# Kernel optimization log

Hardware: AMD Instinct MI355X
Metric: run time of the kernel (lower is better)

Reference implementation:

```python
import jax, jax.numpy as jnp
import numpy as np

MAT_MODE = ((0, 1), (0, 2), (1, 2))
VEC_MODE = (2, 1, 0)
DENSITY_SHIFT = -10.0
DISTANCE_SCALE = 25.0


def grid_sample_2d(img, coords):
    # img: [C, H, W]; coords: [N, 2] in [-1, 1], (x indexes W, y indexes H);
    # bilinear, align_corners=True (matches F.grid_sample in the source).
    C, H, W = img.shape
    x = (coords[:, 0] + 1.0) * 0.5 * (W - 1)
    y = (coords[:, 1] + 1.0) * 0.5 * (H - 1)
    x0 = jnp.floor(x)
    y0 = jnp.floor(y)
    wx = x - x0
    wy = y - y0
    x0i = jnp.clip(x0.astype(jnp.int32), 0, W - 1)
    x1i = jnp.clip(x0i + 1, 0, W - 1)
    y0i = jnp.clip(y0.astype(jnp.int32), 0, H - 1)
    y1i = jnp.clip(y0i + 1, 0, H - 1)
    v00 = img[:, y0i, x0i]
    v01 = img[:, y0i, x1i]
    v10 = img[:, y1i, x0i]
    v11 = img[:, y1i, x1i]
    return (v00 * (1 - wx) * (1 - wy) + v01 * wx * (1 - wy)
            + v10 * (1 - wx) * wy + v11 * wx * wy)  # [C, N]


def line_sample_1d(line, t):
    # line: [C, L]; t: [N] in [-1, 1]. Equivalent to the source's grid_sample on a
    # [1, C, L, 1] tensor with coords (0, t): the width dim (size 1) collapses.
    C, L = line.shape
    y = (t + 1.0) * 0.5 * (L - 1)
    y0 = jnp.floor(y)
    wy = y - y0
    y0i = jnp.clip(y0.astype(jnp.int32), 0, L - 1)
    y1i = jnp.clip(y0i + 1, 0, L - 1)
    return line[:, y0i] * (1 - wy) + line[:, y1i] * wy  # [C, N]


def tensorf_features(planes, lines, xyz):
    # planes: [3, C, H, W]; lines: [3, C, L]; xyz: [N, 3] normalized coords.
    # fusion_two='concat' then fusion_one='multiply' == per-plane multiply, concat.
    feats = []
    for i in range(3):
        a, b = MAT_MODE[i]
        pc = jnp.stack([xyz[:, a], xyz[:, b]], axis=-1)  # [N, 2]
        pf = grid_sample_2d(planes[i], pc)               # [C, N]
        lf = line_sample_1d(lines[i], xyz[:, VEC_MODE[i]])  # [C, N]
        feats.append(pf * lf)
    return jnp.concatenate(feats, axis=0)  # [3C, N]


def raw2alpha(sigma, dist):
    # sigma, dist: [Nr, Ns]
    alpha = 1.0 - jnp.exp(-sigma * dist)
    T = jnp.cumprod(jnp.concatenate(
        [jnp.ones((alpha.shape[0], 1), alpha.dtype), 1.0 - alpha + 1e-10], axis=-1), axis=-1)
    weights = alpha * T[:, :-1]
    return alpha, weights, T[:, -1:]


def setup_inputs() -> dict:
    key = jax.random.key(0)
    ks = jax.random.split(key, 10)
    Nr, Ns, G = 4096, 256, 300
    aabb = jnp.array([[-1.5, -1.5, -1.5], [1.5, 1.5, 1.5]], jnp.float32)
    xyz_sampled = jax.random.uniform(ks[0], (Nr, Ns, 3), jnp.float32,
                                     minval=-1.5, maxval=1.5)
    vd = jax.random.normal(ks[1], (Nr, 3), jnp.float32)
    viewdirs = vd / jnp.linalg.norm(vd, axis=-1, keepdims=True)
    near, far = 2.0, 6.0
    t = jnp.linspace(0.0, 1.0, Ns, dtype=jnp.float32)
    z_vals = near * (1.0 - t) + far * t
    z_vals = jnp.broadcast_to(z_vals, (Nr, Ns)) + \
        jax.random.uniform(ks[2], (Nr, Ns), jnp.float32) * ((far - near) / Ns)
    z_vals = jnp.sort(z_vals, axis=-1)
    s = 0.1  # init_scale
    return {
        'xyz_sampled': xyz_sampled,
        'viewdirs': viewdirs,
        'z_vals': z_vals,
        'density_planes': s * jax.random.normal(ks[3], (3, 8, G, G), jnp.float32),
        'density_lines': s * jax.random.normal(ks[4], (3, 8, G), jnp.float32),
        'app_planes': s * jax.random.normal(ks[5], (3, 24, G, G), jnp.float32),
        'app_lines': s * jax.random.normal(ks[6], (3, 24, G), jnp.float32),
        'density_basis_w': jnp.ones((1, 24), jnp.float32),  # source inits to 1/density_dim
        'app_basis_w': s * jax.random.normal(ks[7], (3, 72), jnp.float32),
        'aabb': aabb,
    }


def reference(xyz_sampled, viewdirs, z_vals, density_planes, density_lines,
              app_planes, app_lines, density_basis_w, app_basis_w, aabb):
    Nr, Ns, _ = xyz_sampled.shape
    # normalize_coord: map aabb -> [-1, 1]
    inv_size = 2.0 / (aabb[1] - aabb[0])
    xyz = ((xyz_sampled - aabb[0]) * inv_size - 1.0).reshape(-1, 3)  # [N, 3]

    dfeat = tensorf_features(density_planes, density_lines, xyz)      # [24, N]
    sigma_feat = (density_basis_w @ dfeat).reshape(Nr, Ns)            # basis_mat
    sigma = jax.nn.softplus(sigma_feat + DENSITY_SHIFT)               # fea2denseAct

    # ray-marching distances
    dists = z_vals[:, 1:] - z_vals[:, :-1]
    dists = jnp.concatenate([dists, dists[:, -1:]], axis=-1)
    alpha, weights, bg_T = raw2alpha(sigma, dists * DISTANCE_SCALE)

    # appearance branch: RGBRender is identity on the 3-dim basis output
    afeat = tensorf_features(app_planes, app_lines, xyz)              # [72, N]
    rgb = (app_basis_w @ afeat).T.reshape(Nr, Ns, 3)

    rgb_map = jnp.sum(weights[..., None] * rgb, axis=1)               # [Nr, 3]
    return rgb_map
```

## Files before the change

### kernel.cpp

```cpp
#include <hip/hip_runtime.h>
#include <math.h>

#define G  300
#define NS 256
#define NR 4096
#define CT 32

typedef _Float16 half16_t;
typedef _Float16 h8 __attribute__((ext_vector_type(8)));

__global__ __launch_bounds__(256) void prep_planes(
    const float* __restrict__ dp, const float* __restrict__ ap,
    half16_t* __restrict__ out)
{
  int t = blockIdx.x * blockDim.x + threadIdx.x;
  if (t >= 3 * G * G) return;
  int x  = t % G;
  int yi = t / G;
  int y  = yi % G;
  int i  = yi / G;
  const float* dpp = dp + ((size_t)(i * 8) * G + y) * G + x;
  const float* app = ap + ((size_t)(i * 24) * G + y) * G + x;
  h8 v[4];
#pragma unroll
  for (int c = 0; c < 8; ++c) v[c >> 3][c & 7] = (half16_t)dpp[(size_t)c * G * G];
#pragma unroll
  for (int c = 0; c < 24; ++c) {
    int cc = c + 8;
    v[cc >> 3][cc & 7] = (half16_t)app[(size_t)c * G * G];
  }
  h8* o = (h8*)(out + (size_t)t * CT);
#pragma unroll
  for (int m = 0; m < 4; ++m) o[m] = v[m];
}

__global__ __launch_bounds__(256) void prep_lines(
    const float* __restrict__ dl, const float* __restrict__ al,
    half16_t* __restrict__ out)
{
  int t = blockIdx.x * blockDim.x + threadIdx.x;
  if (t >= 3 * G) return;
  int p = t % G;
  int i = t / G;
  h8 v[4];
#pragma unroll
  for (int c = 0; c < 8; ++c) v[c >> 3][c & 7] = (half16_t)dl[(i * 8 + c) * G + p];
#pragma unroll
  for (int c = 0; c < 24; ++c) {
    int cc = c + 8;
    v[cc >> 3][cc & 7] = (half16_t)al[(i * 24 + c) * G + p];
  }
  h8* o = (h8*)(out + (size_t)t * CT);
#pragma unroll
  for (int m = 0; m < 4; ++m) o[m] = v[m];
}

__global__ __launch_bounds__(256) void tensorf_fused(
    const float* __restrict__ xyz, const float* __restrict__ zv,
    const half16_t* __restrict__ planes, const half16_t* __restrict__ lns,
    const float* __restrict__ dbw, const float* __restrict__ abw,
    const float* __restrict__ aabb, float* __restrict__ out)
{
  __shared__ float4 srgb[4][NS];

  const int wv   = threadIdx.x >> 6;
  const int lane = threadIdx.x & 63;
  const int ray  = (blockIdx.x << 2) + wv;
  const int q    = lane >> 2;
  const int r    = lane & 3;

  float W[3][24];
  if (r == 0) {
#pragma unroll
    for (int m = 0; m < 24; ++m) { W[0][m] = dbw[m]; W[1][m] = 0.f; W[2][m] = 0.f; }
  } else {
#pragma unroll
    for (int j = 0; j < 3; ++j)
#pragma unroll
      for (int i = 0; i < 3; ++i)
#pragma unroll
        for (int k = 0; k < 8; ++k)
          W[j][i * 8 + k] = abw[j * 72 + i * 24 + (r - 1) * 8 + k];
  }

  const float a0x = aabb[0], a0y = aabb[1], a0z = aabb[2];
  const float ivx = 2.f / (aabb[3] - aabb[0]);
  const float ivy = 2.f / (aabb[4] - aabb[1]);
  const float ivz = 2.f / (aabb[5] - aabb[2]);

  const int MA[3] = {0, 0, 1};
  const int MB[3] = {1, 2, 2};
  const int MV[3] = {2, 1, 0};

  const int ro = r * 8;

  for (int it = 0; it < NS / 16; ++it) {
    int s = it * 16 + q;
    const float* xp = xyz + ((size_t)ray * NS + s) * 3;
    float g[3];
    g[0] = (xp[0] - a0x) * ivx - 1.f;
    g[1] = (xp[1] - a0y) * ivy - 1.f;
    g[2] = (xp[2] - a0z) * ivz - 1.f;

    float acc0 = 0.f, acc1 = 0.f, acc2 = 0.f;
#pragma unroll
    for (int i = 0; i < 3; ++i) {
      float fx = (g[MA[i]] + 1.f) * (0.5f * (G - 1));
      float fy = (g[MB[i]] + 1.f) * (0.5f * (G - 1));
      float ft = (g[MV[i]] + 1.f) * (0.5f * (G - 1));
      float x0f = floorf(fx), y0f = floorf(fy), t0f = floorf(ft);
      float wx = fx - x0f, wy = fy - y0f, wt = ft - t0f;
      int x0 = min(max((int)x0f, 0), G - 1);
      int y0 = min(max((int)y0f, 0), G - 1);
      int t0 = min(max((int)t0f, 0), G - 1);
      int x1 = min(x0 + 1, G - 1);
      int y1 = min(y0 + 1, G - 1);
      int t1 = min(t0 + 1, G - 1);

      const half16_t* pb = planes + (size_t)i * G * G * CT;
      h8 t00 = *(const h8*)(pb + ((size_t)(y0 * G + x0)) * CT + ro);
      h8 t01 = *(const h8*)(pb + ((size_t)(y0 * G + x1)) * CT + ro);
      h8 t10 = *(const h8*)(pb + ((size_t)(y1 * G + x0)) * CT + ro);
      h8 t11 = *(const h8*)(pb + ((size_t)(y1 * G + x1)) * CT + ro);
      const half16_t* lb = lns + (size_t)i * G * CT + ro;
      h8 l0 = *(const h8*)(lb + (size_t)t0 * CT);
      h8 l1 = *(const h8*)(lb + (size_t)t1 * CT);

      float w00 = (1.f - wx) * (1.f - wy), w01 = wx * (1.f - wy);
      float w10 = (1.f - wx) * wy,         w11 = wx * wy;
      float wl0 = 1.f - wt;
#pragma unroll
      for (int k = 0; k < 8; ++k) {
        float pf = (float)t00[k] * w00 + (float)t01[k] * w01
                 + (float)t10[k] * w10 + (float)t11[k] * w11;
        float lf = (float)l0[k] * wl0 + (float)l1[k] * wt;
        float f  = pf * lf;
        acc0 += W[0][i * 8 + k] * f;
        acc1 += W[1][i * 8 + k] * f;
        acc2 += W[2][i * 8 + k] * f;
      }
    }
    float4 v;
    v.x = (r == 0) ? acc0 : 0.f;
    v.y = (r == 0) ? 0.f : acc0;
    v.z = (r == 0) ? 0.f : acc1;
    v.w = (r == 0) ? 0.f : acc2;
#pragma unroll
    for (int m = 1; m <= 2; m <<= 1) {
      v.x += __shfl_xor(v.x, m);
      v.y += __shfl_xor(v.y, m);
      v.z += __shfl_xor(v.z, m);
      v.w += __shfl_xor(v.w, m);
    }
    if (r == 0) srgb[wv][s] = v;
  }
  __syncthreads();

  const float* zp = zv + (size_t)ray * NS + lane * 4;
  float4 z4 = *(const float4*)zp;
  float znext = __shfl_down(z4.x, 1);
  float d[4];
  d[0] = z4.y - z4.x;
  d[1] = z4.z - z4.y;
  d[2] = z4.w - z4.z;
  d[3] = (lane == 63) ? d[2] : (znext - z4.w);

  float4 c[4];
  float al[4];
  float tl = 1.f;
#pragma unroll
  for (int j = 0; j < 4; ++j) {
    c[j] = srgb[wv][lane * 4 + j];
    float vs = c[j].x - 10.0f;
    float sp = (vs > 0.f) ? (vs + log1pf(expf(-vs))) : log1pf(expf(vs));
    al[j] = 1.f - expf(-sp * (d[j] * 25.0f));
    tl *= (1.f - al[j] + 1e-10f);
  }
  float incl = tl;
#pragma unroll
  for (int off = 1; off < 64; off <<= 1) {
    float p = __shfl_up(incl, off);
    if (lane >= off) incl *= p;
  }
  float T = __shfl_up(incl, 1);
  if (lane == 0) T = 1.f;

  float ar = 0.f, ag = 0.f, ab = 0.f;
#pragma unroll
  for (int j = 0; j < 4; ++j) {
    float w = al[j] * T;
    ar += w * c[j].y;
    ag += w * c[j].z;
    ab += w * c[j].w;
    T *= (1.f - al[j] + 1e-10f);
  }
#pragma unroll
  for (int off = 32; off > 0; off >>= 1) {
    ar += __shfl_down(ar, off);
    ag += __shfl_down(ag, off);
    ab += __shfl_down(ab, off);
  }
  if (lane == 0) {
    out[ray * 3 + 0] = ar;
    out[ray * 3 + 1] = ag;
    out[ray * 3 + 2] = ab;
  }
}

extern "C" void kernel_launch(void* const* d_in, const int* in_sizes, int n_in,
                              void* d_out, int out_size, void* d_ws, size_t ws_size,
                              hipStream_t stream)
{
  const float* xyz  = (const float*)d_in[0];
  const float* zv   = (const float*)d_in[2];
  const float* dp   = (const float*)d_in[3];
  const float* dl   = (const float*)d_in[4];
  const float* ap   = (const float*)d_in[5];
  const float* al   = (const float*)d_in[6];
  const float* dbw  = (const float*)d_in[7];
  const float* abw  = (const float*)d_in[8];
  const float* aabb = (const float*)d_in[9];
  float* out = (float*)d_out;

  half16_t* planes16 = (half16_t*)d_ws;
  half16_t* lines16  = planes16 + (size_t)3 * G * G * CT;

  hipLaunchKernelGGL(prep_planes, dim3((3 * G * G + 255) / 256), dim3(256), 0, stream,
                     dp, ap, planes16);
  hipLaunchKernelGGL(prep_lines, dim3((3 * G + 255) / 256), dim3(256), 0, stream,
                     dl, al, lines16);
  hipLaunchKernelGGL(tensorf_fused, dim3(NR / 4), dim3(256), 0, stream,
                     xyz, zv, planes16, lines16, dbw, abw, aabb, out);
}
```

Baseline: 237.8 us.

## Split rays across two waves, move basis weights to LDS, merge prep kernels

The two prep kernels are merged into one launch. The main kernel now assigns each ray to two wavefronts, each covering half the samples, and doubles the grid. The 72-float per-thread basis weight array moves into shared memory to cut register pressure, with a launch-bounds occupancy hint added. The transmittance scan is stitched across the two halves through shared memory, which costs extra block barriers and LDS traffic.

```diff
diff --git a/kernel.cpp b/kernel.cpp
--- a/kernel.cpp
+++ b/kernel.cpp
@@ -9,79 +9,78 @@
 typedef _Float16 half16_t;
 typedef _Float16 h8 __attribute__((ext_vector_type(8)));
 
-__global__ __launch_bounds__(256) void prep_planes(
+__global__ __launch_bounds__(256) void prep_all(
     const float* __restrict__ dp, const float* __restrict__ ap,
-    half16_t* __restrict__ out)
+    const float* __restrict__ dl, const float* __restrict__ al,
+    half16_t* __restrict__ outp, half16_t* __restrict__ outl)
 {
   int t = blockIdx.x * blockDim.x + threadIdx.x;
-  if (t >= 3 * G * G) return;
-  int x  = t % G;
-  int yi = t / G;
-  int y  = yi % G;
-  int i  = yi / G;
-  const float* dpp = dp + ((size_t)(i * 8) * G + y) * G + x;
-  const float* app = ap + ((size_t)(i * 24) * G + y) * G + x;
-  h8 v[4];
-#pragma unroll
-  for (int c = 0; c < 8; ++c) v[c >> 3][c & 7] = (half16_t)dpp[(size_t)c * G * G];
-#pragma unroll
-  for (int c = 0; c < 24; ++c) {
-    int cc = c + 8;
-    v[cc >> 3][cc & 7] = (half16_t)app[(size_t)c * G * G];
-  }
-  h8* o = (h8*)(out + (size_t)t * CT);
-#pragma unroll
-  for (int m = 0; m < 4; ++m) o[m] = v[m];
+  if (t < 3 * G * G) {
+    int x  = t % G;
+    int yi = t / G;
+    int y  = yi % G;
+    int i  = yi / G;
+    const float* dpp = dp + ((size_t)(i * 8) * G + y) * G + x;
+    const float* app = ap + ((size_t)(i * 24) * G + y) * G + x;
+    h8 v[4];
+#pragma unroll
+    for (int c = 0; c < 8; ++c) v[c >> 3][c & 7] = (half16_t)dpp[(size_t)c * G * G];
+#pragma unroll
+    for (int c = 0; c < 24; ++c) {
+      int cc = c + 8;
+      v[cc >> 3][cc & 7] = (half16_t)app[(size_t)c * G * G];
+    }
+    h8* o = (h8*)(outp + (size_t)t * CT);
+#pragma unroll
+    for (int m = 0; m < 4; ++m) o[m] = v[m];
+  } else {
+    int u = t - 3 * G * G;
+    if (u < 3 * G) {
+      int p = u % G;
+      int i = u / G;
+      h8 v[4];
+#pragma unroll
+      for (int c = 0; c < 8; ++c) v[c >> 3][c & 7] = (half16_t)dl[(i * 8 + c) * G + p];
+#pragma unroll
+      for (int c = 0; c < 24; ++c) {
+        int cc = c + 8;
+        v[cc >> 3][cc & 7] = (half16_t)al[(i * 24 + c) * G + p];
+      }
+      h8* o = (h8*)(outl + (size_t)u * CT);
+#pragma unroll
+      for (int m = 0; m < 4; ++m) o[m] = v[m];
+    }
+  }
 }
 
-__global__ __launch_bounds__(256) void prep_lines(
-    const float* __restrict__ dl, const float* __restrict__ al,
-    half16_t* __restrict__ out)
-{
-  int t = blockIdx.x * blockDim.x + threadIdx.x;
-  if (t >= 3 * G) return;
-  int p = t % G;
-  int i = t / G;
-  h8 v[4];
-#pragma unroll
-  for (int c = 0; c < 8; ++c) v[c >> 3][c & 7] = (half16_t)dl[(i * 8 + c) * G + p];
-#pragma unroll
-  for (int c = 0; c < 24; ++c) {
-    int cc = c + 8;
-    v[cc >> 3][cc & 7] = (half16_t)al[(i * 24 + c) * G + p];
-  }
-  h8* o = (h8*)(out + (size_t)t * CT);
-#pragma unroll
-  for (int m = 0; m < 4; ++m) o[m] = v[m];
-}
-
-__global__ __launch_bounds__(256) void tensorf_fused(
+__global__ __launch_bounds__(256, 7) void tensorf_fused(
     const float* __restrict__ xyz, const float* __restrict__ zv,
     const half16_t* __restrict__ planes, const half16_t* __restrict__ lns,
     const float* __restrict__ dbw, const float* __restrict__ abw,
     const float* __restrict__ aabb, float* __restrict__ out)
 {
-  __shared__ float4 srgb[4][NS];
-
-  const int wv   = threadIdx.x >> 6;
-  const int lane = threadIdx.x & 63;
-  const int ray  = (blockIdx.x << 2) + wv;
+  __shared__ float4 srgb[2][NS];
+  __shared__ float  sW[3][128];
+  __shared__ float  sTot[2];
+  __shared__ float4 sSum[2][2];
+
+  const int tid = threadIdx.x;
+  for (int idx = tid; idx < 3 * 128; idx += 256) {
+    int j = idx >> 7, c = idx & 127;
+    float v = 0.f;
+    if (c < 72) v = abw[j * 72 + c];
+    else if (j == 0 && c < 96) v = dbw[c - 72];
+    sW[j][c] = v;
+  }
+  __syncthreads();
+
+  const int wv   = tid >> 6;
+  const int lane = tid & 63;
+  const int rl   = wv >> 1;
+  const int hf   = wv & 1;
+  const int ray  = (blockIdx.x << 1) + rl;
   const int q    = lane >> 2;
   const int r    = lane & 3;
-
-  float W[3][24];
-  if (r == 0) {
-#pragma unroll
-    for (int m = 0; m < 24; ++m) { W[0][m] = dbw[m]; W[1][m] = 0.f; W[2][m] = 0.f; }
-  } else {
-#pragma unroll
-    for (int j = 0; j < 3; ++j)
-#pragma unroll
-      for (int i = 0; i < 3; ++i)
-#pragma unroll
-        for (int k = 0; k < 8; ++k)
-          W[j][i * 8 + k] = abw[j * 72 + i * 24 + (r - 1) * 8 + k];
-  }
 
   const float a0x = aabb[0], a0y = aabb[1], a0z = aabb[2];
   const float ivx = 2.f / (aabb[3] - aabb[0]);
@@ -94,8 +93,8 @@
 
   const int ro = r * 8;
 
-  for (int it = 0; it < NS / 16; ++it) {
-    int s = it * 16 + q;
+  for (int it = 0; it < 8; ++it) {
+    int s = (hf << 7) + (it << 4) + q;
     const float* xp = xyz + ((size_t)ray * NS + s) * 3;
     float g[3];
     g[0] = (xp[0] - a0x) * ivx - 1.f;
@@ -129,16 +128,30 @@
       float w00 = (1.f - wx) * (1.f - wy), w01 = wx * (1.f - wy);
       float w10 = (1.f - wx) * wy,         w11 = wx * wy;
       float wl0 = 1.f - wt;
+
+      float f[8];
 #pragma unroll
       for (int k = 0; k < 8; ++k) {
         float pf = (float)t00[k] * w00 + (float)t01[k] * w01
                  + (float)t10[k] * w10 + (float)t11[k] * w11;
         float lf = (float)l0[k] * wl0 + (float)l1[k] * wt;
-        float f  = pf * lf;
-        acc0 += W[0][i * 8 + k] * f;
-        acc1 += W[1][i * 8 + k] * f;
-        acc2 += W[2][i * 8 + k] * f;
+        f[k] = pf * lf;
       }
+
+      int cb = (r == 0) ? (72 + i * 8) : (i * 24 + (r - 1) * 8);
+      const float4* wp0 = (const float4*)&sW[0][cb];
+      const float4* wp1 = (const float4*)&sW[1][cb];
+      const float4* wp2 = (const float4*)&sW[2][cb];
+      float4 wa, wb;
+      wa = wp0[0]; wb = wp0[1];
+      acc0 += wa.x * f[0] + wa.y * f[1] + wa.z * f[2] + wa.w * f[3]
+            + wb.x * f[4] + wb.y * f[5] + wb.z * f[6] + wb.w * f[7];
+      wa = wp1[0]; wb = wp1[1];
+      acc1 += wa.x * f[0] + wa.y * f[1] + wa.z * f[2] + wa.w * f[3]
+            + wb.x * f[4] + wb.y * f[5] + wb.z * f[6] + wb.w * f[7];
+      wa = wp2[0]; wb = wp2[1];
+      acc2 += wa.x * f[0] + wa.y * f[1] + wa.z * f[2] + wa.w * f[3]
+            + wb.x * f[4] + wb.y * f[5] + wb.z * f[6] + wb.w * f[7];
     }
     float4 v;
     v.x = (r == 0) ? acc0 : 0.f;
@@ -152,58 +165,65 @@
       v.z += __shfl_xor(v.z, m);
       v.w += __shfl_xor(v.w, m);
     }
-    if (r == 0) srgb[wv][s] = v;
-  }
-  __syncthreads();
-
-  const float* zp = zv + (size_t)ray * NS + lane * 4;
-  float4 z4 = *(const float4*)zp;
-  float znext = __shfl_down(z4.x, 1);
-  float d[4];
-  d[0] = z4.y - z4.x;
-  d[1] = z4.z - z4.y;
-  d[2] = z4.w - z4.z;
-  d[3] = (lane == 63) ? d[2] : (znext - z4.w);
-
-  float4 c[4];
-  float al[4];
-  float tl = 1.f;
-#pragma unroll
-  for (int j = 0; j < 4; ++j) {
-    c[j] = srgb[wv][lane * 4 + j];
-    float vs = c[j].x - 10.0f;
-    float sp = (vs > 0.f) ? (vs + log1pf(expf(-vs))) : log1pf(expf(vs));
-    al[j] = 1.f - expf(-sp * (d[j] * 25.0f));
-    tl *= (1.f - al[j] + 1e-10f);
-  }
+    if (r == 0) srgb[rl][s] = v;
+  }
+  __syncthreads();
+
+  const int s0 = (hf << 7) + (lane << 1);
+  const float* zp = zv + (size_t)ray * NS + s0;
+  float2 z2 = *(const float2*)zp;
+  float d0 = z2.y - z2.x;
+  float d1 = (s0 + 2 < NS) ? (zp[2] - z2.y) : d0;
+
+  float4 c0 = srgb[rl][s0];
+  float4 c1 = srgb[rl][s0 + 1];
+
+  float vs0 = c0.x - 10.0f;
+  float sp0 = (vs0 > 0.f) ? (vs0 + log1pf(expf(-vs0))) : log1pf(expf(vs0));
+  float al0 = 1.f - expf(-sp0 * (d0 * 25.0f));
+  float vs1 = c1.x - 10.0f;
+  float sp1 = (vs1 > 0.f) ? (vs1 + log1pf(expf(-vs1))) : log1pf(expf(vs1));
+  float al1 = 1.f - expf(-sp1 * (d1 * 25.0f));
+
+  float tl = (1.f - al0 + 1e-10f) * (1.f - al1 + 1e-10f);
+
   float incl = tl;
 #pragma unroll
   for (int off = 1; off < 64; off <<= 1) {
     float p = __shfl_up(incl, off);
     if (lane >= off) incl *= p;
   }
-  float T = __shfl_up(incl, 1);
-  if (lane == 0) T = 1.f;
-
-  float ar = 0.f, ag = 0.f, ab = 0.f;
-#pragma unroll
-  for (int j = 0; j < 4; ++j) {
-    float w = al[j] * T;
-    ar += w * c[j].y;
-    ag += w * c[j].z;
-    ab += w * c[j].w;
-    T *= (1.f - al[j] + 1e-10f);
-  }
+  float Twave = __shfl_up(incl, 1);
+  if (lane == 0) Twave = 1.f;
+
+  if (hf == 0 && lane == 63) sTot[rl] = incl;
+  __syncthreads();
+
+  float Tstart = hf ? sTot[rl] : 1.f;
+  float T = Tstart * Twave;
+
+  float w0 = al0 * T;
+  T *= (1.f - al0 + 1e-10f);
+  float w1 = al1 * T;
+
+  float ar = w0 * c0.y + w1 * c1.y;
+  float ag = w0 * c0.z + w1 * c1.z;
+  float ab = w0 * c0.w + w1 * c1.w;
 #pragma unroll
   for (int off = 32; off > 0; off >>= 1) {
     ar += __shfl_down(ar, off);
     ag += __shfl_down(ag, off);
     ab += __shfl_down(ab, off);
   }
-  if (lane == 0) {
-    out[ray * 3 + 0] = ar;
-    out[ray * 3 + 1] = ag;
-    out[ray * 3 + 2] = ab;
+  if (lane == 0) sSum[rl][hf] = make_float4(ar, ag, ab, 0.f);
+  __syncthreads();
+
+  if (hf == 0 && lane == 0) {
+    float4 A = sSum[rl][0];
+    float4 B = sSum[rl][1];
+    out[ray * 3 + 0] = A.x + B.x;
+    out[ray * 3 + 1] = A.y + B.y;
+    out[ray * 3 + 2] = A.z + B.z;
   }
 }
 
@@ -225,10 +245,8 @@
   half16_t* planes16 = (half16_t*)d_ws;
   half16_t* lines16  = planes16 + (size_t)3 * G * G * CT;
 
-  hipLaunchKernelGGL(prep_planes, dim3((3 * G * G + 255) / 256), dim3(256), 0, stream,
-                     dp, ap, planes16);
-  hipLaunchKernelGGL(prep_lines, dim3((3 * G + 255) / 256), dim3(256), 0, stream,
-                     dl, al, lines16);
-  hipLaunchKernelGGL(tensorf_fused, dim3(NR / 4), dim3(256), 0, stream,
+  hipLaunchKernelGGL(prep_all, dim3((3 * G * G + 3 * G + 255) / 256), dim3(256), 0, stream,
+                     dp, ap, dl, al, planes16, lines16);
+  hipLaunchKernelGGL(tensorf_fused, dim3(NR / 2), dim3(256), 0, stream,
                      xyz, zv, planes16, lines16, dbw, abw, aabb, out);
 }
```

Result: slower. 795.5 us (+234.5%).

## Bucket samples into plane row slabs per ray to improve gather locality

Applied to the files above, without the earlier changes.

Each wavefront now sorts its ray's samples into row slabs of each plane, using ballot and popcount into shared-memory lists. It then processes the samples plane by plane and slab by slab, accumulating partial features into shared memory. The aim is to make concurrent gathers across waves hit nearby plane rows and improve cache reuse. This costs sorting overhead, extra LDS traffic, read-modify-write accumulation and uneven loop trip counts. The change also merges the two prep kernels into one launch and moves basis weights into shared memory.

```diff
diff --git a/kernel.cpp b/kernel.cpp
--- a/kernel.cpp
+++ b/kernel.cpp
@@ -5,54 +5,53 @@
 #define NS 256
 #define NR 4096
 #define CT 32
+#define SLABS 4
 
 typedef _Float16 half16_t;
 typedef _Float16 h8 __attribute__((ext_vector_type(8)));
 
-__global__ __launch_bounds__(256) void prep_planes(
+__global__ __launch_bounds__(256) void prep_all(
     const float* __restrict__ dp, const float* __restrict__ ap,
-    half16_t* __restrict__ out)
+    const float* __restrict__ dl, const float* __restrict__ al,
+    half16_t* __restrict__ outp, half16_t* __restrict__ outl)
 {
   int t = blockIdx.x * blockDim.x + threadIdx.x;
-  if (t >= 3 * G * G) return;
-  int x  = t % G;
-  int yi = t / G;
-  int y  = yi % G;
-  int i  = yi / G;
-  const float* dpp = dp + ((size_t)(i * 8) * G + y) * G + x;
-  const float* app = ap + ((size_t)(i * 24) * G + y) * G + x;
-  h8 v[4];
-#pragma unroll
-  for (int c = 0; c < 8; ++c) v[c >> 3][c & 7] = (half16_t)dpp[(size_t)c * G * G];
-#pragma unroll
-  for (int c = 0; c < 24; ++c) {
-    int cc = c + 8;
-    v[cc >> 3][cc & 7] = (half16_t)app[(size_t)c * G * G];
-  }
-  h8* o = (h8*)(out + (size_t)t * CT);
-#pragma unroll
-  for (int m = 0; m < 4; ++m) o[m] = v[m];
-}
-
-__global__ __launch_bounds__(256) void prep_lines(
-    const float* __restrict__ dl, const float* __restrict__ al,
-    half16_t* __restrict__ out)
-{
-  int t = blockIdx.x * blockDim.x + threadIdx.x;
-  if (t >= 3 * G) return;
-  int p = t % G;
-  int i = t / G;
-  h8 v[4];
-#pragma unroll
-  for (int c = 0; c < 8; ++c) v[c >> 3][c & 7] = (half16_t)dl[(i * 8 + c) * G + p];
-#pragma unroll
-  for (int c = 0; c < 24; ++c) {
-    int cc = c + 8;
-    v[cc >> 3][cc & 7] = (half16_t)al[(i * 24 + c) * G + p];
-  }
-  h8* o = (h8*)(out + (size_t)t * CT);
-#pragma unroll
-  for (int m = 0; m < 4; ++m) o[m] = v[m];
+  if (t < 3 * G * G) {
+    int x  = t % G;
+    int yi = t / G;
+    int y  = yi % G;
+    int i  = yi / G;
+    const float* dpp = dp + ((size_t)(i * 8) * G + y) * G + x;
+    const float* app = ap + ((size_t)(i * 24) * G + y) * G + x;
+    h8 v[4];
+#pragma unroll
+    for (int c = 0; c < 8; ++c) v[c >> 3][c & 7] = (half16_t)dpp[(size_t)c * G * G];
+#pragma unroll
+    for (int c = 0; c < 24; ++c) {
+      int cc = c + 8;
+      v[cc >> 3][cc & 7] = (half16_t)app[(size_t)c * G * G];
+    }
+    h8* o = (h8*)(outp + (size_t)t * CT);
+#pragma unroll
+    for (int m = 0; m < 4; ++m) o[m] = v[m];
+  } else {
+    int u = t - 3 * G * G;
+    if (u < 3 * G) {
+      int p = u % G;
+      int i = u / G;
+      h8 v[4];
+#pragma unroll
+      for (int c = 0; c < 8; ++c) v[c >> 3][c & 7] = (half16_t)dl[(i * 8 + c) * G + p];
+#pragma unroll
+      for (int c = 0; c < 24; ++c) {
+        int cc = c + 8;
+        v[cc >> 3][cc & 7] = (half16_t)al[(i * 24 + c) * G + p];
+      }
+      h8* o = (h8*)(outl + (size_t)u * CT);
+#pragma unroll
+      for (int m = 0; m < 4; ++m) o[m] = v[m];
+    }
+  }
 }
 
 __global__ __launch_bounds__(256) void tensorf_fused(
@@ -62,101 +61,162 @@
     const float* __restrict__ aabb, float* __restrict__ out)
 {
   __shared__ float4 srgb[4][NS];
-
-  const int wv   = threadIdx.x >> 6;
-  const int lane = threadIdx.x & 63;
+  __shared__ unsigned char lst[4][2][SLABS][NS];
+  __shared__ float sW[3][128];
+
+  const int tid = threadIdx.x;
+  for (int idx = tid; idx < 3 * 128; idx += 256) {
+    int j = idx >> 7, c = idx & 127;
+    float v = 0.f;
+    if (c < 72) v = abw[j * 72 + c];
+    else if (j == 0 && c < 96) v = dbw[c - 72];
+    sW[j][c] = v;
+  }
+
+  const int wv   = tid >> 6;
+  const int lane = tid & 63;
   const int ray  = (blockIdx.x << 2) + wv;
   const int q    = lane >> 2;
   const int r    = lane & 3;
 
-  float W[3][24];
-  if (r == 0) {
-#pragma unroll
-    for (int m = 0; m < 24; ++m) { W[0][m] = dbw[m]; W[1][m] = 0.f; W[2][m] = 0.f; }
-  } else {
-#pragma unroll
-    for (int j = 0; j < 3; ++j)
-#pragma unroll
-      for (int i = 0; i < 3; ++i)
-#pragma unroll
-        for (int k = 0; k < 8; ++k)
-          W[j][i * 8 + k] = abw[j * 72 + i * 24 + (r - 1) * 8 + k];
-  }
+#pragma unroll
+  for (int j = 0; j < 4; ++j) srgb[wv][(lane << 2) + j] = make_float4(0.f, 0.f, 0.f, 0.f);
 
   const float a0x = aabb[0], a0y = aabb[1], a0z = aabb[2];
   const float ivx = 2.f / (aabb[3] - aabb[0]);
   const float ivy = 2.f / (aabb[4] - aabb[1]);
   const float ivz = 2.f / (aabb[5] - aabb[2]);
+  const float A0[3] = {a0x, a0y, a0z};
+  const float IV[3] = {ivx, ivy, ivz};
+
+  __syncthreads();
+
+  int o0[SLABS] = {0, 0, 0, 0};
+  int o1[SLABS] = {0, 0, 0, 0};
+  {
+    const float slabScale = (float)SLABS / (float)G;
+    int key0[4], key1[4];
+#pragma unroll
+    for (int j = 0; j < 4; ++j) {
+      int s = (lane << 2) + j;
+      const float* xp = xyz + ((size_t)ray * NS + s) * 3;
+      float g1 = (xp[1] - a0y) * ivy - 1.f;
+      float g2 = (xp[2] - a0z) * ivz - 1.f;
+      float fy0 = (g1 + 1.f) * (0.5f * (G - 1));
+      float fy1 = (g2 + 1.f) * (0.5f * (G - 1));
+      key0[j] = min(max((int)(fy0 * slabScale), 0), SLABS - 1);
+      key1[j] = min(max((int)(fy1 * slabScale), 0), SLABS - 1);
+    }
+    const unsigned long long ltmask = (1ull << lane) - 1ull;
+#pragma unroll
+    for (int j = 0; j < 4; ++j) {
+      int s = (lane << 2) + j;
+#pragma unroll
+      for (int k = 0; k < SLABS; ++k) {
+        unsigned long long m0 = __ballot(key0[j] == k);
+        if (key0[j] == k)
+          lst[wv][0][k][o0[k] + __popcll(m0 & ltmask)] = (unsigned char)s;
+        o0[k] += (int)__popcll(m0);
+        unsigned long long m1 = __ballot(key1[j] == k);
+        if (key1[j] == k)
+          lst[wv][1][k][o1[k] + __popcll(m1 & ltmask)] = (unsigned char)s;
+        o1[k] += (int)__popcll(m1);
+      }
+    }
+  }
+  __syncthreads();
 
   const int MA[3] = {0, 0, 1};
   const int MB[3] = {1, 2, 2};
   const int MV[3] = {2, 1, 0};
-
   const int ro = r * 8;
 
-  for (int it = 0; it < NS / 16; ++it) {
-    int s = it * 16 + q;
-    const float* xp = xyz + ((size_t)ray * NS + s) * 3;
-    float g[3];
-    g[0] = (xp[0] - a0x) * ivx - 1.f;
-    g[1] = (xp[1] - a0y) * ivy - 1.f;
-    g[2] = (xp[2] - a0z) * ivz - 1.f;
-
-    float acc0 = 0.f, acc1 = 0.f, acc2 = 0.f;
-#pragma unroll
-    for (int i = 0; i < 3; ++i) {
-      float fx = (g[MA[i]] + 1.f) * (0.5f * (G - 1));
-      float fy = (g[MB[i]] + 1.f) * (0.5f * (G - 1));
-      float ft = (g[MV[i]] + 1.f) * (0.5f * (G - 1));
-      float x0f = floorf(fx), y0f = floorf(fy), t0f = floorf(ft);
-      float wx = fx - x0f, wy = fy - y0f, wt = ft - t0f;
-      int x0 = min(max((int)x0f, 0), G - 1);
-      int y0 = min(max((int)y0f, 0), G - 1);
-      int t0 = min(max((int)t0f, 0), G - 1);
-      int x1 = min(x0 + 1, G - 1);
-      int y1 = min(y0 + 1, G - 1);
-      int t1 = min(t0 + 1, G - 1);
-
-      const half16_t* pb = planes + (size_t)i * G * G * CT;
-      h8 t00 = *(const h8*)(pb + ((size_t)(y0 * G + x0)) * CT + ro);
-      h8 t01 = *(const h8*)(pb + ((size_t)(y0 * G + x1)) * CT + ro);
-      h8 t10 = *(const h8*)(pb + ((size_t)(y1 * G + x0)) * CT + ro);
-      h8 t11 = *(const h8*)(pb + ((size_t)(y1 * G + x1)) * CT + ro);
-      const half16_t* lb = lns + (size_t)i * G * CT + ro;
-      h8 l0 = *(const h8*)(lb + (size_t)t0 * CT);
-      h8 l1 = *(const h8*)(lb + (size_t)t1 * CT);
-
-      float w00 = (1.f - wx) * (1.f - wy), w01 = wx * (1.f - wy);
-      float w10 = (1.f - wx) * wy,         w11 = wx * wy;
-      float wl0 = 1.f - wt;
-#pragma unroll
-      for (int k = 0; k < 8; ++k) {
-        float pf = (float)t00[k] * w00 + (float)t01[k] * w01
-                 + (float)t10[k] * w10 + (float)t11[k] * w11;
-        float lf = (float)l0[k] * wl0 + (float)l1[k] * wt;
-        float f  = pf * lf;
-        acc0 += W[0][i * 8 + k] * f;
-        acc1 += W[1][i * 8 + k] * f;
-        acc2 += W[2][i * 8 + k] * f;
+#pragma unroll
+  for (int p = 0; p < 3; ++p) {
+    const int li = (p == 0) ? 0 : 1;
+    const half16_t* pb = planes + (size_t)p * G * G * CT;
+    const half16_t* lb = lns + (size_t)p * G * CT + ro;
+    const int cb = (r == 0) ? (72 + p * 8) : (p * 24 + (r - 1) * 8);
+    const float4 W0a = *(const float4*)&sW[0][cb];
+    const float4 W0b = *(const float4*)&sW[0][cb + 4];
+    const float4 W1a = *(const float4*)&sW[1][cb];
+    const float4 W1b = *(const float4*)&sW[1][cb + 4];
+    const float4 W2a = *(const float4*)&sW[2][cb];
+    const float4 W2b = *(const float4*)&sW[2][cb + 4];
+
+#pragma unroll
+    for (int sl = 0; sl < SLABS; ++sl) {
+      const int n = min((li == 0) ? o0[sl] : o1[sl], NS);
+      for (int base = 0; base < n; base += 16) {
+        int e = base + q;
+        if (e < n) {
+          int sid = lst[wv][li][sl][e];
+          const float* xp = xyz + ((size_t)ray * NS + sid) * 3;
+          float ga = (xp[MA[p]] - A0[MA[p]]) * IV[MA[p]] - 1.f;
+          float gb = (xp[MB[p]] - A0[MB[p]]) * IV[MB[p]] - 1.f;
+          float gv = (xp[MV[p]] - A0[MV[p]]) * IV[MV[p]] - 1.f;
+          float fx = (ga + 1.f) * (0.5f * (G - 1));
+          float fy = (gb + 1.f) * (0.5f * (G - 1));
+          float ft = (gv + 1.f) * (0.5f * (G - 1));
+
+          float x0f = floorf(fx), y0f = floorf(fy), t0f = floorf(ft);
+          float wx = fx - x0f, wy = fy - y0f, wt = ft - t0f;
+          int x0 = min(max((int)x0f, 0), G - 1);
+          int y0 = min(max((int)y0f, 0), G - 1);
+          int t0 = min(max((int)t0f, 0), G - 1);
+          int x1 = min(x0 + 1, G - 1);
+          int y1 = min(y0 + 1, G - 1);
+          int t1 = min(t0 + 1, G - 1);
+
+          h8 t00 = *(const h8*)(pb + ((size_t)(y0 * G + x0)) * CT + ro);
+          h8 t01 = *(const h8*)(pb + ((size_t)(y0 * G + x1)) * CT + ro);
+          h8 t10 = *(const h8*)(pb + ((size_t)(y1 * G + x0)) * CT + ro);
+          h8 t11 = *(const h8*)(pb + ((size_t)(y1 * G + x1)) * CT + ro);
+          h8 l0  = *(const h8*)(lb + (size_t)t0 * CT);
+          h8 l1  = *(const h8*)(lb + (size_t)t1 * CT);
+
+          float w00 = (1.f - wx) * (1.f - wy), w01 = wx * (1.f - wy);
+          float w10 = (1.f - wx) * wy,         w11 = wx * wy;
+          float wl0 = 1.f - wt;
+
+          float f[8];
+#pragma unroll
+          for (int k = 0; k < 8; ++k) {
+            float pf = (float)t00[k] * w00 + (float)t01[k] * w01
+                     + (float)t10[k] * w10 + (float)t11[k] * w11;
+            float lf = (float)l0[k] * wl0 + (float)l1[k] * wt;
+            f[k] = pf * lf;
+          }
+          float acc0 = W0a.x * f[0] + W0a.y * f[1] + W0a.z * f[2] + W0a.w * f[3]
+                     + W0b.x * f[4] + W0b.y * f[5] + W0b.z * f[6] + W0b.w * f[7];
+          float acc1 = W1a.x * f[0] + W1a.y * f[1] + W1a.z * f[2] + W1a.w * f[3]
+                     + W1b.x * f[4] + W1b.y * f[5] + W1b.z * f[6] + W1b.w * f[7];
+          float acc2 = W2a.x * f[0] + W2a.y * f[1] + W2a.z * f[2] + W2a.w * f[3]
+                     + W2b.x * f[4] + W2b.y * f[5] + W2b.z * f[6] + W2b.w * f[7];
+
+          float4 v;
+          v.x = (r == 0) ? acc0 : 0.f;
+          v.y = (r == 0) ? 0.f : acc0;
+          v.z = (r == 0) ? 0.f : acc1;
+          v.w = (r == 0) ? 0.f : acc2;
+#pragma unroll
+          for (int m = 1; m <= 2; m <<= 1) {
+            v.x += __shfl_xor(v.x, m);
+            v.y += __shfl_xor(v.y, m);
+            v.z += __shfl_xor(v.z, m);
+            v.w += __shfl_xor(v.w, m);
+          }
+          if (r == 0) {
+            float4 a = srgb[wv][sid];
+            a.x += v.x; a.y += v.y; a.z += v.z; a.w += v.w;
+            srgb[wv][sid] = a;
+          }
+        }
       }
     }
-    float4 v;
-    v.x = (r == 0) ? acc0 : 0.f;
-    v.y = (r == 0) ? 0.f : acc0;
-    v.z = (r == 0) ? 0.f : acc1;
-    v.w = (r == 0) ? 0.f : acc2;
-#pragma unroll
-    for (int m = 1; m <= 2; m <<= 1) {
-      v.x += __shfl_xor(v.x, m);
-      v.y += __shfl_xor(v.y, m);
-      v.z += __shfl_xor(v.z, m);
-      v.w += __shfl_xor(v.w, m);
-    }
-    if (r == 0) srgb[wv][s] = v;
-  }
-  __syncthreads();
-
-  const float* zp = zv + (size_t)ray * NS + lane * 4;
+  }
+
+  const float* zp = zv + (size_t)ray * NS + (lane << 2);
   float4 z4 = *(const float4*)zp;
   float znext = __shfl_down(z4.x, 1);
   float d[4];
@@ -170,7 +230,7 @@
   float tl = 1.f;
 #pragma unroll
   for (int j = 0; j < 4; ++j) {
-    c[j] = srgb[wv][lane * 4 + j];
+    c[j] = srgb[wv][(lane << 2) + j];
     float vs = c[j].x - 10.0f;
     float sp = (vs > 0.f) ? (vs + log1pf(expf(-vs))) : log1pf(expf(vs));
     al[j] = 1.f - expf(-sp * (d[j] * 25.0f));
@@ -179,8 +239,8 @@
   float incl = tl;
 #pragma unroll
   for (int off = 1; off < 64; off <<= 1) {
-    float p = __shfl_up(incl, off);
-    if (lane >= off) incl *= p;
+    float pp = __shfl_up(incl, off);
+    if (lane >= off) incl *= pp;
   }
   float T = __shfl_up(incl, 1);
   if (lane == 0) T = 1.f;
@@ -220,15 +280,13 @@
   const float* dbw  = (const float*)d_in[7];
   const float* abw  = (const float*)d_in[8];
   const float* aabb = (const float*)d_in[9];
-  float* out = (float*)d_out;
+  float* outp = (float*)d_out;
 
   half16_t* planes16 = (half16_t*)d_ws;
   half16_t* lines16  = planes16 + (size_t)3 * G * G * CT;
 
-  hipLaunchKernelGGL(prep_planes, dim3((3 * G * G + 255) / 256), dim3(256), 0, stream,
-                     dp, ap, planes16);
-  hipLaunchKernelGGL(prep_lines, dim3((3 * G + 255) / 256), dim3(256), 0, stream,
-                     dl, al, lines16);
+  hipLaunchKernelGGL(prep_all, dim3((3 * G * G + 3 * G + 255) / 256), dim3(256), 0, stream,
+                     dp, ap, dl, al, planes16, lines16);
   hipLaunchKernelGGL(tensorf_fused, dim3(NR / 4), dim3(256), 0, stream,
-                     xyz, zv, planes16, lines16, dbw, abw, aabb, out);
+                     xyz, zv, planes16, lines16, dbw, abw, aabb, outp);
 }
```

Result: faster. 220.2 us (-7.4%).
